# Optimization experiments

Hardware: AMD Instinct MI355X
Metric: run time of the kernel (lower is better)

## Reference

```python
import jax, jax.numpy as jnp
import numpy as np

B, S, DIM, H = 4, 1024, 1024, 16
DH = DIM // H
ROPE_THETA = 10000.0


def setup_inputs() -> dict:
    key = jax.random.key(0)
    ks = jax.random.split(key, 9)
    sc = 1.0 / np.sqrt(DIM)
    return {
        "x": jax.random.normal(ks[0], (B, S, DIM), dtype=jnp.float32),
        "Wq": jax.random.normal(ks[1], (DIM, DIM), dtype=jnp.float32) * sc,
        "bq": jax.random.normal(ks[2], (DIM,), dtype=jnp.float32) * 0.02,
        "Wk": jax.random.normal(ks[3], (DIM, DIM), dtype=jnp.float32) * sc,
        "bk": jax.random.normal(ks[4], (DIM,), dtype=jnp.float32) * 0.02,
        "Wv": jax.random.normal(ks[5], (DIM, DIM), dtype=jnp.float32) * sc,
        "bv": jax.random.normal(ks[6], (DIM,), dtype=jnp.float32) * 0.02,
        "Wo": jax.random.normal(ks[7], (DIM, DIM), dtype=jnp.float32) * sc,
        "bo": jax.random.normal(ks[8], (DIM,), dtype=jnp.float32) * 0.02,
    }


def _rope(x):
    # x: (B, S, H, DH). Equinox RotaryPositionalEmbedding (GPT-NeoX half-split style):
    # out = x * tile(cos, 2) + rotate_half(x) * tile(sin, 2)
    seq, d = x.shape[1], x.shape[-1]
    half = d // 2
    freqs = 1.0 / (ROPE_THETA ** (jnp.arange(0, d, 2, dtype=jnp.float32)[:half] / d))  # (half,)
    ang = jnp.outer(jnp.arange(seq, dtype=jnp.float32), freqs)  # (S, half)
    cos = jnp.tile(jnp.cos(ang), (1, 2))[None, :, None, :]  # (1, S, 1, d)
    sin = jnp.tile(jnp.sin(ang), (1, 2))[None, :, None, :]
    x1, x2 = jnp.split(x, 2, axis=-1)
    rot = jnp.concatenate((-x2, x1), axis=-1)  # rotate_half
    return x * cos + rot * sin


def reference(x, Wq, bq, Wk, bk, Wv, bv, Wo, bo):
    # Projections (eqx.nn.Linear: y = W @ x + b, W is (out, in))
    q = (jnp.einsum("bsd,ed->bse", x, Wq) + bq).reshape(B, S, H, DH)
    k = (jnp.einsum("bsd,ed->bse", x, Wk) + bk).reshape(B, S, H, DH)
    v = (jnp.einsum("bsd,ed->bse", x, Wv) + bv).reshape(B, S, H, DH)
    # RoPE on query/key heads (process_heads)
    q = _rope(q)
    k = _rope(k)
    # Scaled dot-product attention, no mask, inference mode
    logits = jnp.einsum("bqhd,bkhd->bhqk", q, k) / jnp.sqrt(jnp.float32(DH))
    w = jax.nn.softmax(logits, axis=-1)
    o = jnp.einsum("bhqk,bkhd->bqhd", w, v).reshape(B, S, DIM)
    return jnp.einsum("bsd,ed->bse", o, Wo) + bo
```

## Files before the change

kernel.cpp:

```cpp
#include <hip/hip_runtime.h>
#include <math.h>

#define B_   4
#define S_   1024
#define DIM_ 1024
#define H_   16
#define DH_  64
#define M_   (B_ * S_)
#define K_   1024

typedef __attribute__((ext_vector_type(8))) short bf16x8;
typedef __attribute__((ext_vector_type(4))) float f32x4;
#define MFMA16(a, b, c) __builtin_amdgcn_mfma_f32_16x16x32_bf16((a), (b), (c), 0, 0, 0)

__device__ __forceinline__ ushort f2bf(float f) {
    union { float f; unsigned u; } v; v.f = f;
    unsigned r = v.u + 0x7FFF + ((v.u >> 16) & 1);
    return (ushort)(r >> 16);
}

__device__ __forceinline__ unsigned pk_bf(float a, float b) {
    union { float f; unsigned u; } x, y; x.f = a; y.f = b;
    return __builtin_amdgcn_perm(y.u + 0x8000u, x.u + 0x8000u, 0x07060302u);
}

__device__ __forceinline__ void gload16(const void* g, void* lds) {
    __builtin_amdgcn_global_load_lds(
        (const __attribute__((address_space(1))) unsigned int*)g,
        (__attribute__((address_space(3))) unsigned int*)lds, 16, 0, 0);
}

__global__ __launch_bounds__(256) void conv_kernel(
    const float* __restrict__ x,  const float* __restrict__ Wq,
    const float* __restrict__ Wk, const float* __restrict__ Wv,
    const float* __restrict__ Wo,
    ushort* __restrict__ Xb, ushort* __restrict__ Wb, ushort* __restrict__ Wob)
{
    const int idx = blockIdx.x * 256 + threadIdx.x;
    const float4* src;
    ushort* dst;
    if (idx < 1048576) {
        src = reinterpret_cast<const float4*>(x) + idx;
        dst = Xb + (size_t)idx * 4;
    } else {
        const int w = idx - 1048576;
        const int which = w >> 18;
        const int off = w & 262143;
        const float* s = (which == 0) ? Wq : (which == 1) ? Wk : (which == 2) ? Wv : Wo;
        src = reinterpret_cast<const float4*>(s) + off;
        dst = (which < 3) ? (Wb + (size_t)which * 1048576 + (size_t)off * 4)
                          : (Wob + (size_t)off * 4);
    }
    float4 v = *src;
    ushort4 o;
    o.x = f2bf(v.x); o.y = f2bf(v.y); o.z = f2bf(v.z); o.w = f2bf(v.w);
    *reinterpret_cast<ushort4*>(dst) = o;
}

__global__ __launch_bounds__(256) void rope_table_kernel(float* __restrict__ cosT,
                                                         float* __restrict__ sinT)
{
    const int idx = blockIdx.x * 256 + threadIdx.x;
    const int s = idx >> 5, j = idx & 31;
    const float freq = powf(10000.0f, -(float)j * (1.0f / 32.0f));
    float sn, cs;
    sincosf((float)s * freq, &sn, &cs);
    cosT[idx] = cs;
    sinT[idx] = sn;
}

__global__ __launch_bounds__(256) void qkv_mfma_kernel(
    const ushort* __restrict__ Xb, const ushort* __restrict__ Wb,
    const float* __restrict__ bq, const float* __restrict__ bk,
    const float* __restrict__ bv,
    const float* __restrict__ cosT, const float* __restrict__ sinT,
    ushort* __restrict__ Qh, ushort* __restrict__ Ksw, ushort* __restrict__ Vsw)
{
    __shared__ ushort As[64 * 64];
    __shared__ ushort Bs[128 * 64];

    const int tid  = threadIdx.x;
    const int wave = tid >> 6;
    const int lane = tid & 63;
    const int l15  = lane & 15;
    const int quad = lane >> 4;
    const int m0   = blockIdx.y * 64;
    const int n0   = blockIdx.x * 128;

    const int h8 = lane >> 3;
    const int c8 = (lane & 7) ^ h8;
    const ushort* Aga = Xb + (size_t)(m0 + h8) * K_ + c8 * 8;
    const ushort* Bga = Wb + (size_t)(n0 + h8) * K_ + c8 * 8;
    const int xr = l15 & 7;

    f32x4 acc[2][4];
    #pragma unroll
    for (int i = 0; i < 2; i++)
        #pragma unroll
        for (int j = 0; j < 4; j++) acc[i][j] = (f32x4){0.f, 0.f, 0.f, 0.f};

    for (int k0 = 0; k0 < K_; k0 += 64) {
        __syncthreads();
        #pragma unroll
        for (int j = 0; j < 2; j++)
            gload16(Aga + (size_t)(wave * 16 + j * 8) * K_ + k0,
                    As + (wave * 2 + j) * 512 + lane * 8);
        #pragma unroll
        for (int j = 0; j < 4; j++)
            gload16(Bga + (size_t)(wave * 32 + j * 8) * K_ + k0,
                    Bs + (wave * 4 + j) * 512 + lane * 8);
        __syncthreads();

        #pragma unroll
        for (int s = 0; s < 2; s++) {
            const int kc = ((s * 4 + quad) ^ xr) * 8;
            bf16x8 af[2], bf[4];
            #pragma unroll
            for (int mi = 0; mi < 2; mi++)
                af[mi] = *reinterpret_cast<const bf16x8*>(
                    As + ((wave & 1) * 32 + mi * 16 + l15) * 64 + kc);
            #pragma unroll
            for (int nj = 0; nj < 4; nj++)
                bf[nj] = *reinterpret_cast<const bf16x8*>(
                    Bs + ((wave >> 1) * 64 + nj * 16 + l15) * 64 + kc);
            #pragma unroll
            for (int mi = 0; mi < 2; mi++)
                #pragma unroll
                for (int nj = 0; nj < 4; nj++)
                    acc[mi][nj] = MFMA16(af[mi], bf[nj], acc[mi][nj]);
        }
    }

    const int zone = n0 >> 10;
    const int nl0  = n0 & 1023;
    const int n_base = nl0 + (wave >> 1) * 64 + l15;
    const int h = (nl0 + (wave >> 1) * 64) >> 6;
    const int r_m0 = m0 + (wave & 1) * 32 + quad * 4;

    if (zone < 2) {
        const float* bias = zone ? bk : bq;
        const float qsc = zone ? 1.0f : 0.125f;
        float bias_l[4];
        #pragma unroll
        for (int ni = 0; ni < 4; ni++) bias_l[ni] = bias[n_base + ni * 16];
        #pragma unroll
        for (int mi = 0; mi < 2; mi++)
            #pragma unroll
            for (int r = 0; r < 4; r++) {
                const int m = r_m0 + mi * 16 + r;
                const int b = m >> 10, s = m & 1023;
                const float cs0 = cosT[s * 32 + l15],      sn0 = sinT[s * 32 + l15];
                const float cs1 = cosT[s * 32 + 16 + l15], sn1 = sinT[s * 32 + 16 + l15];
                ushort* qrow = Qh + ((size_t)(b * H_ + h) * S_ + s) * DH_;
                const size_t kbase = (size_t)(b * H_ + h) * 65536 +
                                     (size_t)(s >> 4) * 1024 + (s & 15) * 8;
                #pragma unroll
                for (int ni = 0; ni < 4; ni++) {
                    const float c = acc[mi][ni][r] + bias_l[ni];
                    const float p = acc[mi][ni ^ 2][r] + bias_l[ni ^ 2];
                    const float cs = (ni & 1) ? cs1 : cs0;
                    const float sn = (ni & 1) ? sn1 : sn0;
                    const float val = (ni & 2) ? fmaf(p, sn, c * cs) : fmaf(-p, sn, c * cs);
                    if (zone == 0) {
                        qrow[ni * 16 + l15] = f2bf(val * qsc);
                    } else {
                        const int dh = ni * 16 + l15;
                        Ksw[kbase + (dh >> 5) * 512 + ((dh >> 3) & 3) * 128 + (dh & 7)] = f2bf(val);
                    }
                }
            }
    } else {
        float bias_l[4];
        #pragma unroll
        for (int ni = 0; ni < 4; ni++) bias_l[ni] = bv[n_base + ni * 16];
        #pragma unroll
        for (int mi = 0; mi < 2; mi++)
            #pragma unroll
            for (int r = 0; r < 4; r++) {
                const int m = r_m0 + mi * 16 + r;
                const int b = m >> 10, s = m & 1023;
                const size_t vbase = (size_t)(b * H_ + h) * 65536 +
                                     (size_t)(s >> 5) * 2048 + ((s >> 3) & 3) * 128 + (s & 7);
                #pragma unroll
                for (int ni = 0; ni < 4; ni++)
                    Vsw[vbase + ni * 512 + l15 * 8] = f2bf(acc[mi][ni][r] + bias_l[ni]);
            }
    }
}

__global__ __launch_bounds__(256) void out_mfma_kernel(
    const ushort* __restrict__ Ob, const ushort* __restrict__ Wob,
    const float* __restrict__ bo, float* __restrict__ out)
{
    __shared__ ushort As[64 * 64];
    __shared__ ushort Bs[128 * 64];

    const int tid  = threadIdx.x;
    const int wave = tid >> 6;
    const int lane = tid & 63;
    const int l15  = lane & 15;
    const int quad = lane >> 4;
    const int m0   = blockIdx.y * 64;
    const int n0   = blockIdx.x * 128;

    const int h8 = lane >> 3;
    const int c8 = (lane & 7) ^ h8;
    const ushort* Aga = Ob + (size_t)(m0 + h8) * K_ + c8 * 8;
    const ushort* Bga = Wob + (size_t)(n0 + h8) * K_ + c8 * 8;
    const int xr = l15 & 7;

    f32x4 acc[2][4];
    #pragma unroll
    for (int i = 0; i < 2; i++)
        #pragma unroll
        for (int j = 0; j < 4; j++) acc[i][j] = (f32x4){0.f, 0.f, 0.f, 0.f};

    for (int k0 = 0; k0 < K_; k0 += 64) {
        __syncthreads();
        #pragma unroll
        for (int j = 0; j < 2; j++)
            gload16(Aga + (size_t)(wave * 16 + j * 8) * K_ + k0,
                    As + (wave * 2 + j) * 512 + lane * 8);
        #pragma unroll
        for (int j = 0; j < 4; j++)
            gload16(Bga + (size_t)(wave * 32 + j * 8) * K_ + k0,
                    Bs + (wave * 4 + j) * 512 + lane * 8);
        __syncthreads();

        #pragma unroll
        for (int s = 0; s < 2; s++) {
            const int kc = ((s * 4 + quad) ^ xr) * 8;
            bf16x8 af[2], bf[4];
            #pragma unroll
            for (int mi = 0; mi < 2; mi++)
                af[mi] = *reinterpret_cast<const bf16x8*>(
                    As + ((wave & 1) * 32 + mi * 16 + l15) * 64 + kc);
            #pragma unroll
            for (int nj = 0; nj < 4; nj++)
                bf[nj] = *reinterpret_cast<const bf16x8*>(
                    Bs + ((wave >> 1) * 64 + nj * 16 + l15) * 64 + kc);
            #pragma unroll
            for (int mi = 0; mi < 2; mi++)
                #pragma unroll
                for (int nj = 0; nj < 4; nj++)
                    acc[mi][nj] = MFMA16(af[mi], bf[nj], acc[mi][nj]);
        }
    }

    const int n_base = n0 + (wave >> 1) * 64 + l15;
    float bias_l[4];
    #pragma unroll
    for (int ni = 0; ni < 4; ni++) bias_l[ni] = bo[n_base + ni * 16];
    const int r_m0 = m0 + (wave & 1) * 32 + quad * 4;
    #pragma unroll
    for (int mi = 0; mi < 2; mi++)
        #pragma unroll
        for (int r = 0; r < 4; r++) {
            const int m = r_m0 + mi * 16 + r;
            float* row = out + (size_t)m * DIM_;
            #pragma unroll
            for (int ni = 0; ni < 4; ni++)
                row[n_base + ni * 16] = acc[mi][ni][r] + bias_l[ni];
        }
}

#define LDPK 72

__global__ __launch_bounds__(256) void attn_mfma_kernel(
    const ushort* __restrict__ Qh, const ushort* __restrict__ Ksw,
    const ushort* __restrict__ Vsw, ushort* __restrict__ O)
{
    const int bh = blockIdx.x >> 4;
    const int q0 = (blockIdx.x & 15) * 64;

    __shared__ ushort Ps[4][16 * LDPK];

    const int tid  = threadIdx.x;
    const int wave = tid >> 6;
    const int lane = tid & 63;
    const int l15  = lane & 15;
    const int quad = lane >> 4;

    const ushort* qp = Qh + ((size_t)bh * S_ + q0 + wave * 16 + l15) * DH_;
    const bf16x8 qf0 = *reinterpret_cast<const bf16x8*>(qp + quad * 8);
    const bf16x8 qf1 = *reinterpret_cast<const bf16x8*>(qp + 32 + quad * 8);

    const ushort* Kb = Ksw + (size_t)bh * 65536 + lane * 8;
    const ushort* Vb = Vsw + (size_t)bh * 65536 + lane * 8;
    ushort* pw = &Ps[wave][0];

    f32x4 o_acc[4];
    #pragma unroll
    for (int c = 0; c < 4; c++) o_acc[c] = (f32x4){0.f, 0.f, 0.f, 0.f};
    float rs = 0.f;

    for (int t = 0; t < 16; t++) {
        const ushort* kt = Kb + t * 4096;
        const ushort* vt = Vb + t * 4096;

        f32x4 sc[4];
        #pragma unroll
        for (int c = 0; c < 4; c++) {
            bf16x8 k0 = *reinterpret_cast<const bf16x8*>(kt + c * 1024);
            bf16x8 k1 = *reinterpret_cast<const bf16x8*>(kt + c * 1024 + 512);
            f32x4 s = (f32x4){0.f, 0.f, 0.f, 0.f};
            s = MFMA16(k0, qf0, s);
            s = MFMA16(k1, qf1, s);
            sc[c] = s;
        }

        bf16x8 vf[2][4];
        #pragma unroll
        for (int j = 0; j < 2; j++)
            #pragma unroll
            for (int c = 0; c < 4; c++)
                vf[j][c] = *reinterpret_cast<const bf16x8*>(vt + j * 2048 + c * 512);

        #pragma unroll
        for (int c = 0; c < 4; c++) {
            const float p0v = __expf(sc[c][0]);
            const float p1v = __expf(sc[c][1]);
            const float p2v = __expf(sc[c][2]);
            const float p3v = __expf(sc[c][3]);
            rs += (p0v + p1v) + (p2v + p3v);
            uint2 pk;
            pk.x = pk_bf(p0v, p1v);
            pk.y = pk_bf(p2v, p3v);
            *reinterpret_cast<uint2*>(pw + l15 * LDPK + c * 16 + quad * 4) = pk;
        }

        const bf16x8 p0 = *reinterpret_cast<const bf16x8*>(pw + l15 * LDPK + quad * 8);
        const bf16x8 p1 = *reinterpret_cast<const bf16x8*>(pw + l15 * LDPK + 32 + quad * 8);
        #pragma unroll
        for (int c = 0; c < 4; c++) {
            o_acc[c] = MFMA16(vf[0][c], p0, o_acc[c]);
            o_acc[c] = MFMA16(vf[1][c], p1, o_acc[c]);
        }
    }

    rs += __shfl_xor(rs, 16, 64);
    rs += __shfl_xor(rs, 32, 64);
    const float inv = 1.0f / rs;

    const int b = bh >> 4, h = bh & 15;
    const int qrow = q0 + wave * 16 + l15;
    ushort* dst = O + ((size_t)(b * S_ + qrow)) * DIM_ + h * 64;
    #pragma unroll
    for (int c = 0; c < 4; c++) {
        uint2 pk;
        pk.x = pk_bf(o_acc[c][0] * inv, o_acc[c][1] * inv);
        pk.y = pk_bf(o_acc[c][2] * inv, o_acc[c][3] * inv);
        *reinterpret_cast<uint2*>(dst + c * 16 + quad * 4) = pk;
    }
}


extern "C" void kernel_launch(void* const* d_in, const int* in_sizes, int n_in,
                              void* d_out, int out_size, void* d_ws, size_t ws_size,
                              hipStream_t stream) {
    const float* x  = (const float*)d_in[0];
    const float* Wq = (const float*)d_in[1];
    const float* bq = (const float*)d_in[2];
    const float* Wk = (const float*)d_in[3];
    const float* bk = (const float*)d_in[4];
    const float* Wv = (const float*)d_in[5];
    const float* bv = (const float*)d_in[6];
    const float* Wo = (const float*)d_in[7];
    const float* bo = (const float*)d_in[8];
    float* out = (float*)d_out;

    const size_t n_elem = (size_t)B_ * S_ * DIM_;
    ushort* Xb  = (ushort*)d_ws;
    ushort* Wb  = Xb + n_elem;
    ushort* Wob = Wb + 3 * 1048576;
    ushort* Qh  = Wob + 1048576;
    ushort* Ksw = Qh + n_elem;
    ushort* Vsw = Ksw + n_elem;
    ushort* Ob  = Vsw + n_elem;
    float* cosT = (float*)(Ob + n_elem);
    float* sinT = cosT + S_ * 32;

    conv_kernel<<<dim3(8192), 256, 0, stream>>>(x, Wq, Wk, Wv, Wo, Xb, Wb, Wob);
    rope_table_kernel<<<dim3(128), 256, 0, stream>>>(cosT, sinT);

    qkv_mfma_kernel<<<dim3(3072 / 128, M_ / 64), 256, 0, stream>>>(
        Xb, Wb, bq, bk, bv, cosT, sinT, Qh, Ksw, Vsw);

    attn_mfma_kernel<<<dim3(B_ * H_ * (S_ / 64)), 256, 0, stream>>>(Qh, Ksw, Vsw, Ob);

    out_mfma_kernel<<<dim3(DIM_ / 128, M_ / 64), 256, 0, stream>>>(Ob, Wob, bo, out);
}
```

Measured before the change: 187.7 us.

## Merge rope table into prep kernel and remap block indices for XCD locality

Folds the RoPE cos/sin table generation into the conversion kernel so one launch does both. The GEMM and attention grids are flattened to 1D, with block indices remapped so that blocks sharing the same N tile or the same batch-head land on the same XCD (blockIdx mod 8), which should improve L2 reuse of weights and K/V. The attention loop over key tiles is also unrolled by 2. The remapping assumes round-robin dispatch of blocks across 8 XCDs, and the unroll may raise register pressure.

```diff
diff --git a/kernel.cpp b/kernel.cpp
--- a/kernel.cpp
+++ b/kernel.cpp
@@ -30,12 +30,23 @@
         (__attribute__((address_space(3))) unsigned int*)lds, 16, 0, 0);
 }
 
-__global__ __launch_bounds__(256) void conv_kernel(
+__global__ __launch_bounds__(256) void prep_kernel(
     const float* __restrict__ x,  const float* __restrict__ Wq,
     const float* __restrict__ Wk, const float* __restrict__ Wv,
     const float* __restrict__ Wo,
-    ushort* __restrict__ Xb, ushort* __restrict__ Wb, ushort* __restrict__ Wob)
+    ushort* __restrict__ Xb, ushort* __restrict__ Wb, ushort* __restrict__ Wob,
+    float* __restrict__ cosT, float* __restrict__ sinT)
 {
+    if (blockIdx.x >= 8192) {
+        const int idx = (blockIdx.x - 8192) * 256 + threadIdx.x;
+        const int s = idx >> 5, j = idx & 31;
+        const float freq = powf(10000.0f, -(float)j * (1.0f / 32.0f));
+        float sn, cs;
+        sincosf((float)s * freq, &sn, &cs);
+        cosT[idx] = cs;
+        sinT[idx] = sn;
+        return;
+    }
     const int idx = blockIdx.x * 256 + threadIdx.x;
     const float4* src;
     ushort* dst;
@@ -57,18 +68,6 @@
     *reinterpret_cast<ushort4*>(dst) = o;
 }
 
-__global__ __launch_bounds__(256) void rope_table_kernel(float* __restrict__ cosT,
-                                                         float* __restrict__ sinT)
-{
-    const int idx = blockIdx.x * 256 + threadIdx.x;
-    const int s = idx >> 5, j = idx & 31;
-    const float freq = powf(10000.0f, -(float)j * (1.0f / 32.0f));
-    float sn, cs;
-    sincosf((float)s * freq, &sn, &cs);
-    cosT[idx] = cs;
-    sinT[idx] = sn;
-}
-
 __global__ __launch_bounds__(256) void qkv_mfma_kernel(
     const ushort* __restrict__ Xb, const ushort* __restrict__ Wb,
     const float* __restrict__ bq, const float* __restrict__ bk,
@@ -84,8 +83,10 @@
     const int lane = tid & 63;
     const int l15  = lane & 15;
     const int quad = lane >> 4;
-    const int m0   = blockIdx.y * 64;
-    const int n0   = blockIdx.x * 128;
+    const int g    = blockIdx.x;
+    const int nt   = (g & 7) * 3 + ((g >> 3) >> 6);
+    const int m0   = ((g >> 3) & 63) * 64;
+    const int n0   = nt * 128;
 
     const int h8 = lane >> 3;
     const int c8 = (lane & 7) ^ h8;
@@ -200,8 +201,9 @@
     const int lane = tid & 63;
     const int l15  = lane & 15;
     const int quad = lane >> 4;
-    const int m0   = blockIdx.y * 64;
-    const int n0   = blockIdx.x * 128;
+    const int g    = blockIdx.x;
+    const int n0   = (g & 7) * 128;
+    const int m0   = (g >> 3) * 64;
 
     const int h8 = lane >> 3;
     const int c8 = (lane & 7) ^ h8;
@@ -270,8 +272,9 @@
     const ushort* __restrict__ Qh, const ushort* __restrict__ Ksw,
     const ushort* __restrict__ Vsw, ushort* __restrict__ O)
 {
-    const int bh = blockIdx.x >> 4;
-    const int q0 = (blockIdx.x & 15) * 64;
+    const int x  = blockIdx.x;
+    const int bh = (x & 7) | ((x >> 7) << 3);
+    const int q0 = ((x >> 3) & 15) * 64;
 
     __shared__ ushort Ps[4][16 * LDPK];
 
@@ -294,6 +297,7 @@
     for (int c = 0; c < 4; c++) o_acc[c] = (f32x4){0.f, 0.f, 0.f, 0.f};
     float rs = 0.f;
 
+    #pragma unroll 2
     for (int t = 0; t < 16; t++) {
         const ushort* kt = Kb + t * 4096;
         const ushort* vt = Vb + t * 4096;
@@ -380,13 +384,13 @@
     float* cosT = (float*)(Ob + n_elem);
     float* sinT = cosT + S_ * 32;
 
-    conv_kernel<<<dim3(8192), 256, 0, stream>>>(x, Wq, Wk, Wv, Wo, Xb, Wb, Wob);
-    rope_table_kernel<<<dim3(128), 256, 0, stream>>>(cosT, sinT);
-
-    qkv_mfma_kernel<<<dim3(3072 / 128, M_ / 64), 256, 0, stream>>>(
+    prep_kernel<<<dim3(8320), 256, 0, stream>>>(x, Wq, Wk, Wv, Wo,
+                                                Xb, Wb, Wob, cosT, sinT);
+
+    qkv_mfma_kernel<<<dim3(1536), 256, 0, stream>>>(
         Xb, Wb, bq, bk, bv, cosT, sinT, Qh, Ksw, Vsw);
 
     attn_mfma_kernel<<<dim3(B_ * H_ * (S_ / 64)), 256, 0, stream>>>(Qh, Ksw, Vsw, Ob);
 
-    out_mfma_kernel<<<dim3(DIM_ / 128, M_ / 64), 256, 0, stream>>>(Ob, Wob, bo, out);
-}
+    out_mfma_kernel<<<dim3(512), 256, 0, stream>>>(Ob, Wob, bo, out);
+}
```

After: 187.3 us. About the same (-0.2%).
